# Optimization experiments

Hardware: AMD Instinct MI355X
Metric: run time of the kernel (lower is better)

Reference implementation:

```python
import jax, jax.numpy as jnp
import numpy as np

N = 100000      # nodes
E = 3200000     # edges (avg degree 32)
IN_C = 256      # input feature dim
HID = 128       # hidden channels (= per-head dim, heads = 1)
L = 3           # num_layers_prop == num_layers_mlp
EPS = 1e-5


def _elu(x):
    return jnp.where(x > 0, x, jnp.expm1(x))


def _bn_eval(x, gamma, beta, mean, var):
    return (x - mean) * jax.lax.rsqrt(var + EPS) * gamma + beta


def _ln(x, gamma, beta):
    mu = jnp.mean(x, axis=-1, keepdims=True)
    var = jnp.var(x, axis=-1, keepdims=True)
    return (x - mu) * jax.lax.rsqrt(var + EPS) * gamma + beta


def setup_inputs() -> dict:
    key = jax.random.key(0)
    ks = jax.random.split(key, 12)
    s_in = np.float32(1.0 / np.sqrt(IN_C))
    s_h = np.float32(1.0 / np.sqrt(HID))
    return {
        "x": jax.random.normal(ks[0], (N, IN_C), jnp.float32),
        "edge_index": jax.random.randint(ks[1], (2, E), 0, N, jnp.int32),
        "mlp_W0": jax.random.normal(ks[2], (IN_C, HID), jnp.float32) * s_in,
        "mlp_b0": jnp.zeros((HID,), jnp.float32),
        "mlp_W": jax.random.normal(ks[3], (L - 1, HID, HID), jnp.float32) * s_h,
        "mlp_b": jnp.zeros((L - 1, HID), jnp.float32),
        "bn_gamma": jnp.ones((L, HID), jnp.float32),
        "bn_beta": jnp.zeros((L, HID), jnp.float32),
        "bn_mean": jnp.zeros((L, HID), jnp.float32),
        "bn_var": jnp.ones((L, HID), jnp.float32),
        "Wq": jax.random.normal(ks[4], (L, HID, HID), jnp.float32) * s_h,
        "bq": jnp.zeros((L, HID), jnp.float32),
        "Wk": jax.random.normal(ks[5], (L, HID, HID), jnp.float32) * s_h,
        "bk": jnp.zeros((L, HID), jnp.float32),
        "Wv": jax.random.normal(ks[6], (L, HID, HID), jnp.float32) * s_h,
        "bv": jnp.zeros((L, HID), jnp.float32),
        "Wg": jax.random.normal(ks[7], (L, HID, HID), jnp.float32) * s_h,
        "bg": jnp.zeros((L, HID), jnp.float32),
        "Wr": jax.random.normal(ks[8], (L, HID, HID), jnp.float32) * s_h,
        "br": jnp.zeros((L, HID), jnp.float32),
        "ln_gamma": jnp.ones((L, HID), jnp.float32),
        "ln_beta": jnp.zeros((L, HID), jnp.float32),
    }


def reference(x, edge_index, mlp_W0, mlp_b0, mlp_W, mlp_b, bn_gamma, bn_beta,
              bn_mean, bn_var, Wq, bq, Wk, bk, Wv, bv, Wg, bg, Wr, br,
              ln_gamma, ln_beta):
    n = x.shape[0]
    # --- mlp_in: Linear -> BN(eval) -> ELU, x3 (dropout p=0 skipped) ---
    h = _elu(_bn_eval(x @ mlp_W0 + mlp_b0, bn_gamma[0], bn_beta[0], bn_mean[0], bn_var[0]))
    for i in range(1, L):
        h = _elu(_bn_eval(h @ mlp_W[i - 1] + mlp_b[i - 1],
                          bn_gamma[i], bn_beta[i], bn_mean[i], bn_var[i]))

    # --- GCN edge normalization (shared across layers) ---
    row, col = edge_index[0], edge_index[1]
    deg = jax.ops.segment_sum(jnp.ones((E,), x.dtype), col, num_segments=n)
    val = jnp.sqrt(1.0 / deg[col]) * jnp.sqrt(1.0 / deg[row])
    val = jnp.nan_to_num(val, nan=0.0, posinf=0.0, neginf=0.0)

    # --- stacked TransConv layers (num_heads = 1) ---
    for i in range(L):
        prev = h
        q = h @ Wq[i] + bq[i]              # [N, M]
        k = h @ Wk[i] + bk[i]              # [N, M]
        v = h @ Wv[i] + bv[i]              # [N, D]
        qn = q / jnp.linalg.norm(q, axis=-1, keepdims=True)
        kn = k / jnp.linalg.norm(k, axis=-1, keepdims=True)
        kvs = kn.T @ v                     # [M, D]
        num = qn @ kvs + jnp.sum(v, axis=0)            # [N, D]
        denom = qn @ jnp.sum(kn, axis=0) + jnp.asarray(n, x.dtype)  # [N]
        attn_out = num / denom[:, None]    # heads=1 -> mean over heads is identity
        # sparse GCN: out[col] += val * gnn_in[row]
        g = h @ Wg[i] + bg[i]
        agg = jax.ops.segment_sum(val[:, None] * g[row], col, num_segments=n)
        out = attn_out + agg + (h @ Wr[i] + br[i])
        out = out + prev                   # outer residual in Transformer.forward
        h = _elu(_ln(out, ln_gamma[i], ln_beta[i]))
    return h
```

## Files before the change

kernel.cpp:

```cpp
#include <hip/hip_runtime.h>
#include <cstdint>
#include <cstddef>

#define HID 128
#define INC 256
#define NLAYER 3
#define SLOTS 96
#define P2G 16

static constexpr float EPS = 1e-5f;

typedef __attribute__((ext_vector_type(8))) short s16x8;
typedef __attribute__((ext_vector_type(4))) unsigned short us16x4;
typedef __attribute__((ext_vector_type(4))) float f32x4;
typedef __attribute__((ext_vector_type(2))) float f32x2;

__device__ __forceinline__ float eluf(float x) { return x > 0.f ? x : expm1f(x); }

__device__ __forceinline__ unsigned short f2bf(float x)
{
    unsigned u = __float_as_uint(x);
    u += 0x7FFFu + ((u >> 16) & 1u);
    return (unsigned short)(u >> 16);
}

__device__ __forceinline__ float bf2f(unsigned short u)
{
    return __uint_as_float(((unsigned)u) << 16);
}

__device__ __forceinline__ unsigned char f2fp8(float x)
{
    return (unsigned char)(__builtin_amdgcn_cvt_pk_fp8_f32(x, x, 0, false) & 0xFF);
}

__device__ __forceinline__ bool csr_side(int hostGrid, const int* __restrict__ ei,
                                         int* cnt, int* crow, int Etot, int e0, int e1)
{
    if ((int)blockIdx.x < hostGrid) return false;
    int e = e0 + (int)(blockIdx.x - hostGrid) * 256 + (int)threadIdx.x;
    if (e < e1) {
        int r = ei[e], c = ei[Etot + e];
        int p = atomicAdd(&cnt[c], 1);
        if (p < SLOTS) crow[(size_t)c * SLOTS + p] = r;
    }
    return true;
}

template<int K, bool IN32>
__global__ __launch_bounds__(256) void gemm_mlp(
    const float* __restrict__ Af, const unsigned short* __restrict__ A16,
    const unsigned short* __restrict__ Wth,
    const float* __restrict__ bias,
    const float* __restrict__ bng, const float* __restrict__ bnb,
    const float* __restrict__ bnm, const float* __restrict__ bnv,
    unsigned short* __restrict__ C16, int n,
    const int* __restrict__ ei, int* cntp, int* crowp, int Etot, int e0, int e1,
    int hostGrid)
{
    if (csr_side(hostGrid, ei, cntp, crowp, Etot, e0, e1)) return;

    __shared__ unsigned short Ah[64 * 64], Wh[128 * 64];
    const int t = threadIdx.x;
    const int l = t & 63;
    const int w = t >> 6;
    const int l15 = l & 15;
    const int row0 = blockIdx.x * 64;

    char* cAh = (char*)Ah;
    char* cWh = (char*)Wh;

    f32x4 acc[8] = {};

    for (int kc = 0; kc < K; kc += 64) {
        if (IN32) {
            #pragma unroll
            for (int i = 0; i < 4; ++i) {
                int f = t + 256 * i;
                int r = f >> 4, c4 = f & 15;
                int gr = row0 + r; if (gr > n - 1) gr = n - 1;
                float4 a4 = *(const float4*)&Af[(size_t)gr * K + kc + c4 * 4];
                int byte = r * 128 + (((c4 >> 1) * 16) ^ ((r & 7) << 4)) + (c4 & 1) * 8;
                *(us16x4*)(cAh + byte) =
                    (us16x4){f2bf(a4.x), f2bf(a4.y), f2bf(a4.z), f2bf(a4.w)};
            }
        } else {
            #pragma unroll
            for (int i = 0; i < 2; ++i) {
                int f = t + 256 * i;
                int r = f >> 3, c8 = f & 7;
                int gr = row0 + r; if (gr > n - 1) gr = n - 1;
                int byte = r * 128 + ((c8 * 16) ^ ((r & 7) << 4));
                *(s16x8*)(cAh + byte) = *(const s16x8*)&A16[(size_t)gr * K + kc + c8 * 8];
            }
        }
        #pragma unroll
        for (int i = 0; i < 4; ++i) {
            int f = t + 256 * i;
            int nr = f >> 3, c8 = f & 7;
            size_t gsrc = (size_t)nr * K + kc + c8 * 8;
            int byte = nr * 128 + ((c8 * 16) ^ ((nr & 7) << 4));
            *(s16x8*)(cWh + byte) = *(const s16x8*)&Wth[gsrc];
        }
        __syncthreads();
        #pragma unroll
        for (int ks = 0; ks < 2; ++ks) {
            int jA = ks * 4 + (l >> 4);
            int ar = w * 16 + l15;
            int aoff = ar * 128 + ((jA * 16) ^ ((ar & 7) << 4));
            s16x8 fah = *(s16x8*)(cAh + aoff);
            #pragma unroll
            for (int nt = 0; nt < 8; ++nt) {
                int nr = nt * 16 + l15;
                int boff = nr * 128 + ((jA * 16) ^ ((nr & 7) << 4));
                acc[nt] = __builtin_amdgcn_mfma_f32_16x16x32_bf16(fah, *(s16x8*)(cWh + boff), acc[nt], 0, 0, 0);
            }
        }
        __syncthreads();
    }

    const int rbase = row0 + w * 16 + ((l >> 4) << 2);
    #pragma unroll
    for (int nt = 0; nt < 8; ++nt) {
        int col = nt * 16 + l15;
        float bb = bias[col];
        float gm = bng[col], bt = bnb[col], mn = bnm[col], vr = bnv[col];
        #pragma unroll
        for (int r = 0; r < 4; ++r) {
            int row = rbase + r;
            if (row < n) {
                float o = acc[nt][r] + bb;
                o = eluf((o - mn) * rsqrtf(vr + EPS) * gm + bt);
                C16[(size_t)row * HID + col] = f2bf(o);
            }
        }
    }
}

struct QKVGRArgs {
    const unsigned short* wh[5];
    const float* bias[5];
};

__global__ __launch_bounds__(256) void fused_qkvgr(
    const unsigned short* __restrict__ A16, QKVGRArgs ar,
    unsigned short* __restrict__ qb16,
    unsigned char* __restrict__ gb8, float* __restrict__ accout,
    unsigned short* __restrict__ partial, int n,
    const int* __restrict__ ei, int* cntp, int* crowp, int Etot, int e0, int e1,
    int hostGrid)
{
    if (csr_side(hostGrid, ei, cntp, crowp, Etot, e0, e1)) return;

    __shared__ char smem[65536];
    char* cA  = smem;
    char* cW  = smem + 16384;
    char* cVT = smem + 49152;

    const int t = threadIdx.x;
    const int l = t & 63;
    const int w = t >> 6;
    const int l15 = l & 15;
    const int row0 = blockIdx.x * 64;

    #pragma unroll
    for (int i = 0; i < 4; ++i) {
        int f = t + 256 * i;
        int r = f >> 4, c8 = f & 15;
        int gr = row0 + r; if (gr > n - 1) gr = n - 1;
        int byte = r * 256 + ((c8 * 16) ^ ((r & 7) << 4));
        *(s16x8*)(cA + byte) = *(const s16x8*)&A16[(size_t)gr * HID + c8 * 8];
    }
    __syncthreads();

    s16x8 fah[4];
    {
        const int arow = w * 16 + l15;
        #pragma unroll
        for (int ks = 0; ks < 4; ++ks) {
            int aoff = arow * 256 + (((ks * 64) + (l >> 4) * 16) ^ ((arow & 7) << 4));
            fah[ks] = *(s16x8*)(cA + aoff);
        }
    }
    __syncthreads();

    const int rbase = row0 + w * 16 + ((l >> 4) << 2);
    const int rtb   = w * 16 + ((l >> 4) << 2);
    float skred[8], svred[8];

    for (int m = 0; m < 5; ++m) {
        {
            const unsigned short* wh = ar.wh[m];
            #pragma unroll
            for (int i = 0; i < 8; ++i) {
                int f = t + 256 * i;
                int nr = f >> 4, c8 = f & 15;
                int byte = nr * 256 + ((c8 * 16) ^ ((nr & 7) << 4));
                *(s16x8*)(cW + byte) = *(const s16x8*)&wh[(size_t)nr * HID + c8 * 8];
            }
        }
        __syncthreads();

        f32x4 acc[8] = {};
        #pragma unroll
        for (int ks = 0; ks < 4; ++ks) {
            #pragma unroll
            for (int nt = 0; nt < 8; ++nt) {
                int nr = nt * 16 + l15;
                int boff = nr * 256 + (((ks * 64) + (l >> 4) * 16) ^ ((nr & 7) << 4));
                acc[nt] = __builtin_amdgcn_mfma_f32_16x16x32_bf16(fah[ks], *(s16x8*)(cW + boff), acc[nt], 0, 0, 0);
            }
        }

        float bb[8];
        #pragma unroll
        for (int nt = 0; nt < 8; ++nt) bb[nt] = ar.bias[m][nt * 16 + l15];

        if (m <= 1) {
            float sk8[8] = {};
            #pragma unroll
            for (int r = 0; r < 4; ++r) {
                float ss = 0.f;
                #pragma unroll
                for (int nt = 0; nt < 8; ++nt) {
                    float o = acc[nt][r] + bb[nt];
                    ss += o * o;
                }
                ss += __shfl_xor(ss, 1); ss += __shfl_xor(ss, 2);
                ss += __shfl_xor(ss, 4); ss += __shfl_xor(ss, 8);
                float rn = rsqrtf(ss);
                int row = rbase + r;
                if (m == 0) {
                    if (row < n) {
                        #pragma unroll
                        for (int nt = 0; nt < 8; ++nt)
                            qb16[(size_t)row * HID + nt * 16 + l15] = f2bf((acc[nt][r] + bb[nt]) * rn);
                    }
                } else {
                    int rt = rtb + r;
                    bool ok = (row < n);
                    #pragma unroll
                    for (int nt = 0; nt < 8; ++nt) {
                        int kd = nt * 16 + l15;
                        float on = (acc[nt][r] + bb[nt]) * rn;
                        unsigned short v16 = ok ? f2bf(on) : (unsigned short)0;
                        int byte = kd * 128 + ((2 * rt) ^ ((kd & 7) << 4));
                        *(unsigned short*)(cA + byte) = v16;
                        sk8[nt] += ok ? on : 0.f;
                    }
                }
            }
            if (m == 1) {
                #pragma unroll
                for (int nt = 0; nt < 8; ++nt) {
                    float s = sk8[nt];
                    s += __shfl_xor(s, 16);
                    s += __shfl_xor(s, 32);
                    skred[nt] = s;
                }
            }
        } else if (m == 2) {
            float sv8[8] = {};
            #pragma unroll
            for (int r = 0; r < 4; ++r) {
                int row = rbase + r;
                int rt = rtb + r;
                bool ok = (row < n);
                #pragma unroll
                for (int nt = 0; nt < 8; ++nt) {
                    int vd = nt * 16 + l15;
                    float on = acc[nt][r] + bb[nt];
                    unsigned short v16 = ok ? f2bf(on) : (unsigned short)0;
                    int byte = vd * 128 + ((2 * rt) ^ ((vd & 7) << 4));
                    *(unsigned short*)(cVT + byte) = v16;
                    sv8[nt] += ok ? on : 0.f;
                }
            }
            #pragma unroll
            for (int nt = 0; nt < 8; ++nt) {
                float s = sv8[nt];
                s += __shfl_xor(s, 16);
                s += __shfl_xor(s, 32);
                svred[nt] = s;
            }
        } else if (m == 3) {
            #pragma unroll
            for (int r = 0; r < 4; ++r) {
                int row = rbase + r;
                if (row < n) {
                    #pragma unroll
                    for (int nt = 0; nt < 8; ++nt)
                        gb8[(size_t)row * HID + nt * 16 + l15] = f2fp8(acc[nt][r] + bb[nt]);
                }
            }
        } else {
            #pragma unroll
            for (int r = 0; r < 4; ++r) {
                int row = rbase + r;
                if (row < n) {
                    #pragma unroll
                    for (int nt = 0; nt < 8; ++nt) {
                        int col = nt * 16 + l15;
                        accout[(size_t)row * HID + col] =
                            acc[nt][r] + bb[nt] + bf2f(A16[(size_t)row * HID + col]);
                    }
                }
            }
        }
        __syncthreads();
    }

    float* sksf = (float*)cW;
    float* svsf = (float*)(cW + 2048);
    if (l < 16) {
        #pragma unroll
        for (int nt = 0; nt < 8; ++nt) {
            sksf[w * 128 + nt * 16 + l15] = skred[nt];
            svsf[w * 128 + nt * 16 + l15] = svred[nt];
        }
    }

    f32x4 kacc[2][8] = {};
    #pragma unroll
    for (int ks = 0; ks < 2; ++ks) {
        #pragma unroll
        for (int mt = 0; mt < 2; ++mt) {
            int kd = w * 32 + mt * 16 + l15;
            int aoff = kd * 128 + ((ks * 64 + (l >> 4) * 16) ^ ((kd & 7) << 4));
            s16x8 fa = *(s16x8*)(cA + aoff);
            #pragma unroll
            for (int nt = 0; nt < 8; ++nt) {
                int vd = nt * 16 + l15;
                int boff = vd * 128 + ((ks * 64 + (l >> 4) * 16) ^ ((vd & 7) << 4));
                kacc[mt][nt] = __builtin_amdgcn_mfma_f32_16x16x32_bf16(fa, *(s16x8*)(cVT + boff), kacc[mt][nt], 0, 0, 0);
            }
        }
    }
    __syncthreads();

    unsigned short* pb = partial + (size_t)blockIdx.x * 16640;
    #pragma unroll
    for (int mt = 0; mt < 2; ++mt) {
        #pragma unroll
        for (int nt = 0; nt < 8; ++nt) {
            #pragma unroll
            for (int r = 0; r < 4; ++r) {
                int kd = w * 32 + mt * 16 + ((l >> 4) << 2) + r;
                pb[kd * 128 + nt * 16 + l15] = f2bf(kacc[mt][nt][r]);
            }
        }
    }
    if (t < 128) {
        pb[16384 + t] = f2bf(sksf[t] + sksf[128 + t] + sksf[256 + t] + sksf[384 + t]);
    } else {
        int vd = t - 128;
        pb[16512 + vd] = f2bf(svsf[vd] + svsf[128 + vd] + svsf[256 + vd] + svsf[384 + vd]);
    }
}

__global__ __launch_bounds__(256) void gemm_num_combine(
    const unsigned short* __restrict__ A16,
    const unsigned short* __restrict__ Bth,
    const float* __restrict__ sumv, const float* __restrict__ snk,
    float nf, float* __restrict__ accio, int n,
    const int* __restrict__ ei, int* cntp, int* crowp, int Etot, int e0, int e1,
    int hostGrid)
{
    if (csr_side(hostGrid, ei, cntp, crowp, Etot, e0, e1)) return;

    __shared__ char smem[16384 + 32768];
    char* cA = smem;
    char* cW = smem + 16384;

    const int t = threadIdx.x;
    const int l = t & 63;
    const int w = t >> 6;
    const int l15 = l & 15;
    const int row0 = blockIdx.x * 64;

    #pragma unroll
    for (int i = 0; i < 4; ++i) {
        int f = t + 256 * i;
        int r = f >> 4, c8 = f & 15;
        int gr = row0 + r; if (gr > n - 1) gr = n - 1;
        int byte = r * 256 + ((c8 * 16) ^ ((r & 7) << 4));
        *(s16x8*)(cA + byte) = *(const s16x8*)&A16[(size_t)gr * HID + c8 * 8];
    }
    #pragma unroll
    for (int i = 0; i < 8; ++i) {
        int f = t + 256 * i;
        int nr = f >> 4, c8 = f & 15;
        int byte = nr * 256 + ((c8 * 16) ^ ((nr & 7) << 4));
        *(s16x8*)(cW + byte) = *(const s16x8*)&Bth[(size_t)nr * HID + c8 * 8];
    }
    __syncthreads();

    f32x4 acc[8] = {};
    const int arow = w * 16 + l15;
    #pragma unroll
    for (int ks = 0; ks < 4; ++ks) {
        int aoff = arow * 256 + (((ks * 64) + (l >> 4) * 16) ^ ((arow & 7) << 4));
        s16x8 fa = *(s16x8*)(cA + aoff);
        #pragma unroll
        for (int nt = 0; nt < 8; ++nt) {
            int nr = nt * 16 + l15;
            int boff = nr * 256 + (((ks * 64) + (l >> 4) * 16) ^ ((nr & 7) << 4));
            acc[nt] = __builtin_amdgcn_mfma_f32_16x16x32_bf16(fa, *(s16x8*)(cW + boff), acc[nt], 0, 0, 0);
        }
    }

    const int rbase = row0 + w * 16 + ((l >> 4) << 2);
    const int rtb   = w * 16 + ((l >> 4) << 2);
    float bb[8], skn[8];
    #pragma unroll
    for (int nt = 0; nt < 8; ++nt) {
        bb[nt]  = sumv[nt * 16 + l15];
        skn[nt] = snk[nt * 16 + l15];
    }
    #pragma unroll
    for (int r = 0; r < 4; ++r) {
        int row = rbase + r;
        int rt = rtb + r;
        float p = 0.f;
        #pragma unroll
        for (int nt = 0; nt < 8; ++nt) {
            int byte = rt * 256 + ((2 * (nt * 16 + l15)) ^ ((rt & 7) << 4));
            p += bf2f(*(unsigned short*)(cA + byte)) * skn[nt];
        }
        p += __shfl_xor(p, 1); p += __shfl_xor(p, 2);
        p += __shfl_xor(p, 4); p += __shfl_xor(p, 8);
        float dinv = 1.f / (p + nf);
        if (row < n) {
            #pragma unroll
            for (int nt = 0; nt < 8; ++nt) {
                size_t idx = (size_t)row * HID + nt * 16 + l15;
                accio[idx] += (acc[nt][r] + bb[nt]) * dinv;
            }
        }
    }
}

struct WConvArgs {
    const float* src[18];
    unsigned short* dh[18];
    int K[18];
};

__global__ void conv_weights(WConvArgs a)
{
    int m = blockIdx.x;
    const float* s = a.src[m];
    unsigned short* dh = a.dh[m];
    int K = a.K[m];
    int tot = 128 * K;
    int slice = (tot + gridDim.y - 1) / gridDim.y;
    int i0 = blockIdx.y * slice;
    int i1 = min(tot, i0 + slice);
    for (int idx = i0 + threadIdx.x; idx < i1; idx += 256) {
        int nn = idx / K, k = idx - nn * K;
        dh[idx] = f2bf(s[(size_t)k * 128 + nn]);
    }
}

__global__ __launch_bounds__(256) void reduce_kvs_p2a(
    const unsigned short* __restrict__ partial, int nb,
    float* __restrict__ partial2)
{
    const int oq = blockIdx.x * 256 + threadIdx.x;
    if (oq >= 4160) return;
    const int g   = blockIdx.y;
    const int per = (nb + P2G - 1) / P2G;
    const int b0  = g * per;
    const int b1  = min(nb, b0 + per);

    float s0 = 0.f, s1 = 0.f, s2 = 0.f, s3 = 0.f;
    int b = b0;
    for (; b + 3 < b1; b += 4) {
        us16x4 u0 = *(const us16x4*)&partial[(size_t)(b + 0) * 16640 + oq * 4];
        us16x4 u1 = *(const us16x4*)&partial[(size_t)(b + 1) * 16640 + oq * 4];
        us16x4 u2 = *(const us16x4*)&partial[(size_t)(b + 2) * 16640 + oq * 4];
        us16x4 u3 = *(const us16x4*)&partial[(size_t)(b + 3) * 16640 + oq * 4];
        s0 += bf2f(u0[0]) + bf2f(u1[0]) + bf2f(u2[0]) + bf2f(u3[0]);
        s1 += bf2f(u0[1]) + bf2f(u1[1]) + bf2f(u2[1]) + bf2f(u3[1]);
        s2 += bf2f(u0[2]) + bf2f(u1[2]) + bf2f(u2[2]) + bf2f(u3[2]);
        s3 += bf2f(u0[3]) + bf2f(u1[3]) + bf2f(u2[3]) + bf2f(u3[3]);
    }
    for (; b < b1; ++b) {
        us16x4 u0 = *(const us16x4*)&partial[(size_t)b * 16640 + oq * 4];
        s0 += bf2f(u0[0]); s1 += bf2f(u0[1]); s2 += bf2f(u0[2]); s3 += bf2f(u0[3]);
    }
    *(f32x4*)&partial2[(size_t)g * 16640 + oq * 4] = (f32x4){s0, s1, s2, s3};
}

__global__ __launch_bounds__(256) void reduce_kvs_p2b(
    const float* __restrict__ partial2,
    unsigned short* __restrict__ kvth, float* __restrict__ sums)
{
    int o = blockIdx.x * 256 + threadIdx.x;
    if (o >= 16640) return;
    float tot = 0.f;
    #pragma unroll
    for (int g = 0; g < P2G; ++g)
        tot += partial2[(size_t)g * 16640 + o];
    if (o < 16384) {
        int k = o >> 7, nn = o & 127;
        kvth[nn * 128 + k] = f2bf(tot);
    } else {
        sums[o - 16384] = tot;
    }
}

__global__ void rdeg_k(const int* __restrict__ cur, float* __restrict__ rdeg, int n)
{
    int i = blockIdx.x * 256 + threadIdx.x;
    if (i < n) {
        int c = cur[i];
        rdeg[i] = (c > 0) ? rsqrtf((float)c) : 0.f;
    }
}

__global__ __launch_bounds__(256) void gather_ln_elu4(
    const int* __restrict__ cnt, const int* __restrict__ crow,
    const float* __restrict__ rdeg,
    const unsigned char* __restrict__ g, const float* __restrict__ accin,
    const float* __restrict__ gam, const float* __restrict__ bet,
    float* __restrict__ outf, unsigned short* __restrict__ out16, int n)
{
    int node = (int)((blockIdx.x * 256 + threadIdx.x) >> 4);
    int li   = threadIdx.x & 15;
    if (node >= n) return;

    int cn = cnt[node]; if (cn > SLOTS) cn = SLOTS;
    const int* cr = &crow[(size_t)node * SLOTS];
    float rd = rdeg[node];
    const unsigned b8 = (unsigned)li * 8u;
    float4 a0 = *(const float4*)&accin[(size_t)node * HID + li * 8];
    float4 a1 = *(const float4*)&accin[(size_t)node * HID + li * 8 + 4];

    auto acc8 = [&](uint2 U_, float W_) {
        f32x2 pa = __builtin_amdgcn_cvt_pk_f32_fp8((int)U_.x, false);
        f32x2 pb = __builtin_amdgcn_cvt_pk_f32_fp8((int)U_.x, true);
        f32x2 pc = __builtin_amdgcn_cvt_pk_f32_fp8((int)U_.y, false);
        f32x2 pd = __builtin_amdgcn_cvt_pk_f32_fp8((int)U_.y, true);
        a0.x += W_ * pa[0]; a0.y += W_ * pa[1];
        a0.z += W_ * pb[0]; a0.w += W_ * pb[1];
        a1.x += W_ * pc[0]; a1.y += W_ * pc[1];
        a1.z += W_ * pd[0]; a1.w += W_ * pd[1];
    };

    int i = 0;
    for (; i + 3 < cn; i += 4) {
        int   r0 = cr[i],     r1 = cr[i + 1];
        int   r2 = cr[i + 2], r3 = cr[i + 3];
        float w0 = rd * rdeg[r0], w1 = rd * rdeg[r1];
        float w2 = rd * rdeg[r2], w3 = rd * rdeg[r3];
        uint2 u0 = *(const uint2*)&g[(unsigned)r0 * 128u + b8];
        uint2 u1 = *(const uint2*)&g[(unsigned)r1 * 128u + b8];
        uint2 u2 = *(const uint2*)&g[(unsigned)r2 * 128u + b8];
        uint2 u3 = *(const uint2*)&g[(unsigned)r3 * 128u + b8];
        acc8(u0, w0); acc8(u1, w1); acc8(u2, w2); acc8(u3, w3);
    }
    for (; i < cn; ++i) {
        int r0 = cr[i];
        float w0 = rd * rdeg[r0];
        uint2 u0 = *(const uint2*)&g[(unsigned)r0 * 128u + b8];
        acc8(u0, w0);
    }

    float sm = a0.x + a0.y + a0.z + a0.w + a1.x + a1.y + a1.z + a1.w;
    float ss = a0.x * a0.x + a0.y * a0.y + a0.z * a0.z + a0.w * a0.w
             + a1.x * a1.x + a1.y * a1.y + a1.z * a1.z + a1.w * a1.w;
    #pragma unroll
    for (int o = 8; o; o >>= 1) { sm += __shfl_xor(sm, o); ss += __shfl_xor(ss, o); }
    float mu  = sm * (1.f / 128.f);
    float var = ss * (1.f / 128.f) - mu * mu;
    float rs  = rsqrtf(var + EPS);
    float4 gm0 = *(const float4*)&gam[li * 8];
    float4 gm1 = *(const float4*)&gam[li * 8 + 4];
    float4 bt0 = *(const float4*)&bet[li * 8];
    float4 bt1 = *(const float4*)&bet[li * 8 + 4];
    float y0 = eluf((a0.x - mu) * rs * gm0.x + bt0.x);
    float y1 = eluf((a0.y - mu) * rs * gm0.y + bt0.y);
    float y2 = eluf((a0.z - mu) * rs * gm0.z + bt0.z);
    float y3 = eluf((a0.w - mu) * rs * gm0.w + bt0.w);
    float y4 = eluf((a1.x - mu) * rs * gm1.x + bt1.x);
    float y5 = eluf((a1.y - mu) * rs * gm1.y + bt1.y);
    float y6 = eluf((a1.z - mu) * rs * gm1.z + bt1.z);
    float y7 = eluf((a1.w - mu) * rs * gm1.w + bt1.w);
    if (out16) {
        us16x4 o0 = (us16x4){f2bf(y0), f2bf(y1), f2bf(y2), f2bf(y3)};
        us16x4 o1 = (us16x4){f2bf(y4), f2bf(y5), f2bf(y6), f2bf(y7)};
        *(us16x4*)&out16[(size_t)node * HID + li * 8]     = o0;
        *(us16x4*)&out16[(size_t)node * HID + li * 8 + 4] = o1;
    } else {
        *(float4*)&outf[(size_t)node * HID + li * 8]     = make_float4(y0, y1, y2, y3);
        *(float4*)&outf[(size_t)node * HID + li * 8 + 4] = make_float4(y4, y5, y6, y7);
    }
}

extern "C" void kernel_launch(void* const* d_in, const int* in_sizes, int n_in,
                              void* d_out, int out_size, void* d_ws, size_t ws_size,
                              hipStream_t stream)
{
    const float* x      = (const float*)d_in[0];
    const int*   ei     = (const int*)  d_in[1];
    const float* mlp_W0 = (const float*)d_in[2];
    const float* mlp_b0 = (const float*)d_in[3];
    const float* mlp_W  = (const float*)d_in[4];
    const float* mlp_b  = (const float*)d_in[5];
    const float* bn_g   = (const float*)d_in[6];
    const float* bn_b   = (const float*)d_in[7];
    const float* bn_m   = (const float*)d_in[8];
    const float* bn_v   = (const float*)d_in[9];
    const float* Wq = (const float*)d_in[10]; const float* bq = (const float*)d_in[11];
    const float* Wk = (const float*)d_in[12]; const float* bk = (const float*)d_in[13];
    const float* Wv = (const float*)d_in[14]; const float* bv = (const float*)d_in[15];
    const float* Wg = (const float*)d_in[16]; const float* bg = (const float*)d_in[17];
    const float* Wr = (const float*)d_in[18]; const float* br = (const float*)d_in[19];
    const float* ln_g = (const float*)d_in[20];
    const float* ln_b = (const float*)d_in[21];

    const int N = in_sizes[0] / INC;
    const int E = in_sizes[1] / 2;
    const size_t P = (size_t)N * HID;
    const int gemmGrid = (N + 63) / 64;

    unsigned short* partial = (unsigned short*)d_ws;
    size_t partUS = (size_t)gemmGrid * 16640;
    if (partUS < P) partUS = P;
    unsigned short* h16  = partial + partUS;
    unsigned short* qb16 = h16 + P;
    unsigned char*  gb8  = (unsigned char*)(qb16 + P);
    float* kvs  = (float*)(gb8 + P);
    float* partial2 = kvs + 256;
    int*   crow = (int*)(partial2 + (size_t)P2G * 16640);
    int*   cnt  = crow + (size_t)N * SLOTS;
    float* rdeg = (float*)(cnt + N);
    unsigned short* wt = (unsigned short*)(rdeg + N);

    unsigned short* mlpA = partial;
    unsigned short* mlpB = qb16;

    unsigned short* WTh[18];
    int Ks[18];
    size_t woff = 0;
    for (int m = 0; m < 18; ++m) {
        int K = (m == 0) ? INC : HID;
        Ks[m] = K;
        WTh[m] = wt + woff;           woff += (size_t)128 * K;
    }
    unsigned short* kvth = wt + woff; woff += 16384;
    float* acc = (float*)d_out;

    const int gw4Grid  = (N + 15) / 16;
    const int nodeGrid = (N + 255) / 256;

    int eb[6];
    for (int i = 0; i <= 5; ++i) eb[i] = (int)(((long long)E * i) / 5);
    auto cb = [&](int i) { return (eb[i + 1] - eb[i] + 255) / 256; };

    WConvArgs wa;
    const float* srcs[18];
    srcs[0] = mlp_W0; srcs[1] = mlp_W; srcs[2] = mlp_W + (size_t)HID * HID;
    for (int l = 0; l < NLAYER; ++l) {
        const size_t wo = (size_t)l * HID * HID;
        srcs[3 + l * 5 + 0] = Wq + wo;
        srcs[3 + l * 5 + 1] = Wk + wo;
        srcs[3 + l * 5 + 2] = Wv + wo;
        srcs[3 + l * 5 + 3] = Wg + wo;
        srcs[3 + l * 5 + 4] = Wr + wo;
    }
    for (int m = 0; m < 18; ++m) {
        wa.src[m] = srcs[m]; wa.dh[m] = WTh[m]; wa.K[m] = Ks[m];
    }
    conv_weights<<<dim3(18, 8), 256, 0, stream>>>(wa);

    hipMemsetAsync(cnt, 0, (size_t)N * sizeof(int), stream);

    gemm_mlp<INC, true><<<gemmGrid + cb(0), 256, 0, stream>>>(x, nullptr, WTh[0], mlp_b0,
        bn_g, bn_b, bn_m, bn_v, mlpA, N, ei, cnt, crow, E, eb[0], eb[1], gemmGrid);
    gemm_mlp<HID, false><<<gemmGrid + cb(1), 256, 0, stream>>>(nullptr, mlpA, WTh[1], mlp_b,
        bn_g + HID, bn_b + HID, bn_m + HID, bn_v + HID, mlpB, N,
        ei, cnt, crow, E, eb[1], eb[2], gemmGrid);
    gemm_mlp<HID, false><<<gemmGrid + cb(2), 256, 0, stream>>>(nullptr, mlpB, WTh[2], mlp_b + HID,
        bn_g + 2 * HID, bn_b + 2 * HID, bn_m + 2 * HID, bn_v + 2 * HID, h16, N,
        ei, cnt, crow, E, eb[2], eb[3], gemmGrid);

    for (int l = 0; l < NLAYER; ++l) {
        const int bo = l * HID;
        const bool l0 = (l == 0);

        QKVGRArgs qa;
        for (int m = 0; m < 5; ++m) qa.wh[m] = WTh[3 + l * 5 + m];
        qa.bias[0] = bq + bo; qa.bias[1] = bk + bo; qa.bias[2] = bv + bo;
        qa.bias[3] = bg + bo; qa.bias[4] = br + bo;

        fused_qkvgr<<<gemmGrid + (l0 ? cb(3) : 0), 256, 0, stream>>>(h16, qa,
            qb16, gb8, acc, partial, N,
            ei, cnt, crow, E, l0 ? eb[3] : 0, l0 ? eb[4] : 0, gemmGrid);

        reduce_kvs_p2a<<<dim3(17, P2G), 256, 0, stream>>>(partial, gemmGrid, partial2);
        reduce_kvs_p2b<<<65, 256, 0, stream>>>(partial2, kvth, kvs);

        gemm_num_combine<<<gemmGrid + (l0 ? cb(4) : 0), 256, 0, stream>>>(qb16, kvth,
            kvs + 128, kvs, (float)N, acc, N,
            ei, cnt, crow, E, l0 ? eb[4] : 0, l0 ? eb[5] : 0, gemmGrid);

        if (l0) rdeg_k<<<nodeGrid, 256, 0, stream>>>(cnt, rdeg, N);

        bool last = (l == NLAYER - 1);
        gather_ln_elu4<<<gw4Grid, 256, 0, stream>>>(cnt, crow, rdeg,
            gb8, acc, ln_g + bo, ln_b + bo,
            last ? acc : nullptr, last ? nullptr : h16, N);
    }
}
```

Baseline: 765.5 us.

## Double fused QKVGR tile to 128 rows with 512-thread blocks

Each fused_qkvgr block now has 512 threads and handles 128 rows instead of 64, using 96KB of dynamic shared memory. Each weight tile is now loaded once per 128 rows, which halves weight staging traffic and halves the number of per-block K^T V partials the reduction kernels must sum. The trade-off is larger LDS use per block, so fewer blocks fit on each CU, and the edge-side CSR blocks are resized to 512 threads to match.

```diff
diff --git a/kernel.cpp b/kernel.cpp
--- a/kernel.cpp
+++ b/kernel.cpp
@@ -34,11 +34,12 @@
     return (unsigned char)(__builtin_amdgcn_cvt_pk_fp8_f32(x, x, 0, false) & 0xFF);
 }
 
+template<int BS>
 __device__ __forceinline__ bool csr_side(int hostGrid, const int* __restrict__ ei,
                                          int* cnt, int* crow, int Etot, int e0, int e1)
 {
     if ((int)blockIdx.x < hostGrid) return false;
-    int e = e0 + (int)(blockIdx.x - hostGrid) * 256 + (int)threadIdx.x;
+    int e = e0 + (int)(blockIdx.x - hostGrid) * BS + (int)threadIdx.x;
     if (e < e1) {
         int r = ei[e], c = ei[Etot + e];
         int p = atomicAdd(&cnt[c], 1);
@@ -58,7 +59,7 @@
     const int* __restrict__ ei, int* cntp, int* crowp, int Etot, int e0, int e1,
     int hostGrid)
 {
-    if (csr_side(hostGrid, ei, cntp, crowp, Etot, e0, e1)) return;
+    if (csr_side<256>(hostGrid, ei, cntp, crowp, Etot, e0, e1)) return;
 
     __shared__ unsigned short Ah[64 * 64], Wh[128 * 64];
     const int t = threadIdx.x;
@@ -142,7 +143,7 @@
     const float* bias[5];
 };
 
-__global__ __launch_bounds__(256) void fused_qkvgr(
+__global__ __launch_bounds__(512) void fused_qkvgr(
     const unsigned short* __restrict__ A16, QKVGRArgs ar,
     unsigned short* __restrict__ qb16,
     unsigned char* __restrict__ gb8, float* __restrict__ accout,
@@ -150,22 +151,22 @@
     const int* __restrict__ ei, int* cntp, int* crowp, int Etot, int e0, int e1,
     int hostGrid)
 {
-    if (csr_side(hostGrid, ei, cntp, crowp, Etot, e0, e1)) return;
-
-    __shared__ char smem[65536];
+    if (csr_side<512>(hostGrid, ei, cntp, crowp, Etot, e0, e1)) return;
+
+    extern __shared__ char smem[];
     char* cA  = smem;
-    char* cW  = smem + 16384;
-    char* cVT = smem + 49152;
+    char* cW  = smem + 32768;
+    char* cVT = smem + 65536;
 
     const int t = threadIdx.x;
     const int l = t & 63;
     const int w = t >> 6;
     const int l15 = l & 15;
-    const int row0 = blockIdx.x * 64;
+    const int row0 = blockIdx.x * 128;
 
     #pragma unroll
     for (int i = 0; i < 4; ++i) {
-        int f = t + 256 * i;
+        int f = t + 512 * i;
         int r = f >> 4, c8 = f & 15;
         int gr = row0 + r; if (gr > n - 1) gr = n - 1;
         int byte = r * 256 + ((c8 * 16) ^ ((r & 7) << 4));
@@ -192,8 +193,8 @@
         {
             const unsigned short* wh = ar.wh[m];
             #pragma unroll
-            for (int i = 0; i < 8; ++i) {
-                int f = t + 256 * i;
+            for (int i = 0; i < 4; ++i) {
+                int f = t + 512 * i;
                 int nr = f >> 4, c8 = f & 15;
                 int byte = nr * 256 + ((c8 * 16) ^ ((nr & 7) << 4));
                 *(s16x8*)(cW + byte) = *(const s16x8*)&wh[(size_t)nr * HID + c8 * 8];
@@ -244,7 +245,7 @@
                         int kd = nt * 16 + l15;
                         float on = (acc[nt][r] + bb[nt]) * rn;
                         unsigned short v16 = ok ? f2bf(on) : (unsigned short)0;
-                        int byte = kd * 128 + ((2 * rt) ^ ((kd & 7) << 4));
+                        int byte = kd * 256 + ((2 * rt) ^ ((kd & 7) << 4));
                         *(unsigned short*)(cA + byte) = v16;
                         sk8[nt] += ok ? on : 0.f;
                     }
@@ -271,7 +272,7 @@
                     int vd = nt * 16 + l15;
                     float on = acc[nt][r] + bb[nt];
                     unsigned short v16 = ok ? f2bf(on) : (unsigned short)0;
-                    int byte = vd * 128 + ((2 * rt) ^ ((vd & 7) << 4));
+                    int byte = vd * 256 + ((2 * rt) ^ ((vd & 7) << 4));
                     *(unsigned short*)(cVT + byte) = v16;
                     sv8[nt] += ok ? on : 0.f;
                 }
@@ -311,7 +312,7 @@
     }
 
     float* sksf = (float*)cW;
-    float* svsf = (float*)(cW + 2048);
+    float* svsf = (float*)(cW + 4096);
     if (l < 16) {
         #pragma unroll
         for (int nt = 0; nt < 8; ++nt) {
@@ -320,19 +321,18 @@
         }
     }
 
-    f32x4 kacc[2][8] = {};
-    #pragma unroll
-    for (int ks = 0; ks < 2; ++ks) {
-        #pragma unroll
-        for (int mt = 0; mt < 2; ++mt) {
-            int kd = w * 32 + mt * 16 + l15;
-            int aoff = kd * 128 + ((ks * 64 + (l >> 4) * 16) ^ ((kd & 7) << 4));
+    f32x4 kacc[8] = {};
+    {
+        int kd = w * 16 + l15;
+        #pragma unroll
+        for (int ks = 0; ks < 4; ++ks) {
+            int aoff = kd * 256 + ((ks * 64 + (l >> 4) * 16) ^ ((kd & 7) << 4));
             s16x8 fa = *(s16x8*)(cA + aoff);
             #pragma unroll
             for (int nt = 0; nt < 8; ++nt) {
                 int vd = nt * 16 + l15;
-                int boff = vd * 128 + ((ks * 64 + (l >> 4) * 16) ^ ((vd & 7) << 4));
-                kacc[mt][nt] = __builtin_amdgcn_mfma_f32_16x16x32_bf16(fa, *(s16x8*)(cVT + boff), kacc[mt][nt], 0, 0, 0);
+                int boff = vd * 256 + ((ks * 64 + (l >> 4) * 16) ^ ((vd & 7) << 4));
+                kacc[nt] = __builtin_amdgcn_mfma_f32_16x16x32_bf16(fa, *(s16x8*)(cVT + boff), kacc[nt], 0, 0, 0);
             }
         }
     }
@@ -340,21 +340,24 @@
 
     unsigned short* pb = partial + (size_t)blockIdx.x * 16640;
     #pragma unroll
-    for (int mt = 0; mt < 2; ++mt) {
-        #pragma unroll
-        for (int nt = 0; nt < 8; ++nt) {
-            #pragma unroll
-            for (int r = 0; r < 4; ++r) {
-                int kd = w * 32 + mt * 16 + ((l >> 4) << 2) + r;
-                pb[kd * 128 + nt * 16 + l15] = f2bf(kacc[mt][nt][r]);
-            }
+    for (int nt = 0; nt < 8; ++nt) {
+        #pragma unroll
+        for (int r = 0; r < 4; ++r) {
+            int kd = w * 16 + ((l >> 4) << 2) + r;
+            pb[kd * 128 + nt * 16 + l15] = f2bf(kacc[nt][r]);
         }
     }
     if (t < 128) {
-        pb[16384 + t] = f2bf(sksf[t] + sksf[128 + t] + sksf[256 + t] + sksf[384 + t]);
-    } else {
+        float s = 0.f;
+        #pragma unroll
+        for (int ww = 0; ww < 8; ++ww) s += sksf[ww * 128 + t];
+        pb[16384 + t] = f2bf(s);
+    } else if (t < 256) {
         int vd = t - 128;
-        pb[16512 + vd] = f2bf(svsf[vd] + svsf[128 + vd] + svsf[256 + vd] + svsf[384 + vd]);
+        float s = 0.f;
+        #pragma unroll
+        for (int ww = 0; ww < 8; ++ww) s += svsf[ww * 128 + vd];
+        pb[16512 + vd] = f2bf(s);
     }
 }
 
@@ -366,11 +369,11 @@
     const int* __restrict__ ei, int* cntp, int* crowp, int Etot, int e0, int e1,
     int hostGrid)
 {
-    if (csr_side(hostGrid, ei, cntp, crowp, Etot, e0, e1)) return;
-
-    __shared__ char smem[16384 + 32768];
-    char* cA = smem;
-    char* cW = smem + 16384;
+    if (csr_side<256>(hostGrid, ei, cntp, crowp, Etot, e0, e1)) return;
+
+    __shared__ char smem2[16384 + 32768];
+    char* cA = smem2;
+    char* cW = smem2 + 16384;
 
     const int t = threadIdx.x;
     const int l = t & 63;
@@ -624,9 +627,10 @@
     const int E = in_sizes[1] / 2;
     const size_t P = (size_t)N * HID;
     const int gemmGrid = (N + 63) / 64;
+    const int qkvGrid  = (N + 127) / 128;
 
     unsigned short* partial = (unsigned short*)d_ws;
-    size_t partUS = (size_t)gemmGrid * 16640;
+    size_t partUS = (size_t)qkvGrid * 16640;
     if (partUS < P) partUS = P;
     unsigned short* h16  = partial + partUS;
     unsigned short* qb16 = h16 + P;
@@ -657,7 +661,8 @@
 
     int eb[6];
     for (int i = 0; i <= 5; ++i) eb[i] = (int)(((long long)E * i) / 5);
-    auto cb = [&](int i) { return (eb[i + 1] - eb[i] + 255) / 256; };
+    auto cb256 = [&](int i) { return (eb[i + 1] - eb[i] + 255) / 256; };
+    auto cb512 = [&](int i) { return (eb[i + 1] - eb[i] + 511) / 512; };
 
     WConvArgs wa;
     const float* srcs[18];
@@ -677,12 +682,12 @@
 
     hipMemsetAsync(cnt, 0, (size_t)N * sizeof(int), stream);
 
-    gemm_mlp<INC, true><<<gemmGrid + cb(0), 256, 0, stream>>>(x, nullptr, WTh[0], mlp_b0,
+    gemm_mlp<INC, true><<<gemmGrid + cb256(0), 256, 0, stream>>>(x, nullptr, WTh[0], mlp_b0,
         bn_g, bn_b, bn_m, bn_v, mlpA, N, ei, cnt, crow, E, eb[0], eb[1], gemmGrid);
-    gemm_mlp<HID, false><<<gemmGrid + cb(1), 256, 0, stream>>>(nullptr, mlpA, WTh[1], mlp_b,
+    gemm_mlp<HID, false><<<gemmGrid + cb256(1), 256, 0, stream>>>(nullptr, mlpA, WTh[1], mlp_b,
         bn_g + HID, bn_b + HID, bn_m + HID, bn_v + HID, mlpB, N,
         ei, cnt, crow, E, eb[1], eb[2], gemmGrid);
-    gemm_mlp<HID, false><<<gemmGrid + cb(2), 256, 0, stream>>>(nullptr, mlpB, WTh[2], mlp_b + HID,
+    gemm_mlp<HID, false><<<gemmGrid + cb256(2), 256, 0, stream>>>(nullptr, mlpB, WTh[2], mlp_b + HID,
         bn_g + 2 * HID, bn_b + 2 * HID, bn_m + 2 * HID, bn_v + 2 * HID, h16, N,
         ei, cnt, crow, E, eb[2], eb[3], gemmGrid);
 
@@ -695,14 +700,14 @@
         qa.bias[0] = bq + bo; qa.bias[1] = bk + bo; qa.bias[2] = bv + bo;
         qa.bias[3] = bg + bo; qa.bias[4] = br + bo;
 
-        fused_qkvgr<<<gemmGrid + (l0 ? cb(3) : 0), 256, 0, stream>>>(h16, qa,
+        fused_qkvgr<<<qkvGrid + (l0 ? cb512(3) : 0), 512, 98304, stream>>>(h16, qa,
             qb16, gb8, acc, partial, N,
-            ei, cnt, crow, E, l0 ? eb[3] : 0, l0 ? eb[4] : 0, gemmGrid);
-
-        reduce_kvs_p2a<<<dim3(17, P2G), 256, 0, stream>>>(partial, gemmGrid, partial2);
+            ei, cnt, crow, E, l0 ? eb[3] : 0, l0 ? eb[4] : 0, qkvGrid);
+
+        reduce_kvs_p2a<<<dim3(17, P2G), 256, 0, stream>>>(partial, qkvGrid, partial2);
         reduce_kvs_p2b<<<65, 256, 0, stream>>>(partial2, kvth, kvs);
 
-        gemm_num_combine<<<gemmGrid + (l0 ? cb(4) : 0), 256, 0, stream>>>(qb16, kvth,
+        gemm_num_combine<<<gemmGrid + (l0 ? cb256(4) : 0), 256, 0, stream>>>(qb16, kvth,
             kvs + 128, kvs, (float)N, acc, N,
             ei, cnt, crow, E, l0 ? eb[4] : 0, l0 ? eb[5] : 0, gemmGrid);
 
```

Measured after the change: 774.1 us. No clear change (+1.1%).
